# Kernel tuning notes

Hardware: AMD Instinct MI355X
Metric: run time of the kernel (lower is better)

Reference implementation:

```python
import jax, jax.numpy as jnp
import numpy as np

B, NC, A, C, G = 8, 6, 25200, 10, 20  # batch, cameras, anchors, classes, GT per camera
MAX_GT = 32                            # padded GT slots per camera (>= max num_gt)
LAMBDA_COORD, LAMBDA_NOOBJ, LAMBDA_OBJ, LAMBDA_CLS = 5.0, 0.5, 1.0, 1.0
IOU_THR = 0.5


def setup_inputs() -> dict:
    key = jax.random.key(0)
    k1, k2, k3, k4, k5, k6, k7 = jax.random.split(key, 7)
    cams = B * NC
    gt_cxcy = jax.random.uniform(k1, (cams * G, 2), minval=0.1, maxval=0.9)
    gt_wh = jax.random.uniform(k2, (cams * G, 2), minval=0.05, maxval=0.3)
    gt_boxes = jnp.concatenate([gt_cxcy, gt_wh], axis=-1)           # (960, 4) cxcywh, normalized
    gt_labels = jax.random.randint(k3, (cams * G,), 0, C)            # (960,)
    # per-sample cumulative end indices: [20, 40, ..., 120] per row
    start_end_idx = jnp.tile((jnp.arange(NC) + 1) * G, (B, 1)).astype(jnp.int32)
    pred_boxes = jax.random.uniform(k4, (cams, A, 4))
    # overlay noisy copies of the GT boxes on the first G anchors so positives exist
    noise = 0.01 * jax.random.normal(k5, (cams, G, 4))
    pred_boxes = pred_boxes.at[:, :G, :].set(gt_boxes.reshape(cams, G, 4) + noise)
    pred_labels = jax.random.normal(k6, (cams, A, C))
    pred_objectness = jax.random.normal(k7, (cams, A, 1))
    return {
        'pred_boxes': pred_boxes,
        'pred_labels': pred_labels,
        'pred_objectness': pred_objectness,
        'gt_boxes': gt_boxes,
        'gt_labels': gt_labels,
        'start_end_idx': start_end_idx,
    }


def _iou_cxcywh(pb, gb):
    # pb: (cams, A, 4), gb: (cams, MG, 4) -> (cams, A, MG)
    p = pb[:, :, None, :]
    g = gb[:, None, :, :]
    p1, p2 = p[..., :2] - p[..., 2:] * 0.5, p[..., :2] + p[..., 2:] * 0.5
    g1, g2 = g[..., :2] - g[..., 2:] * 0.5, g[..., :2] + g[..., 2:] * 0.5
    wh = jnp.clip(jnp.minimum(p2, g2) - jnp.maximum(p1, g1), 0.0)
    inter = wh[..., 0] * wh[..., 1]
    area_p = p[..., 2] * p[..., 3]
    area_g = g[..., 2] * g[..., 3]
    return inter / (area_p + area_g - inter + 1e-6)


def _safe_mean(x, mask):
    # per-camera mean over masked anchors; 0 if mask empty. x, mask: (cams, A)
    cnt = mask.sum(-1)
    s = (x * mask).sum(-1)
    return jnp.where(cnt > 0, s / jnp.maximum(cnt, 1.0), 0.0)


def reference(pred_boxes, pred_labels, pred_objectness, gt_boxes, gt_labels, start_end_idx):
    cams = pred_boxes.shape[0]
    s = start_end_idx.astype(jnp.int32)                              # (B, NC) per-sample cumulative
    offsets = jnp.concatenate([jnp.zeros((1,), jnp.int32), jnp.cumsum(s[:, -1])])[:-1]  # (B,)
    starts = (offsets[:, None] + jnp.concatenate(
        [jnp.zeros((s.shape[0], 1), jnp.int32), s[:, :-1]], axis=1)).reshape(-1)        # (cams,)
    ends = (offsets[:, None] + s).reshape(-1)                        # (cams,)
    ngt = ends - starts                                              # (cams,)

    k = jnp.arange(MAX_GT, dtype=jnp.int32)
    gidx = starts[:, None] + k[None, :]                              # (cams, MG)
    valid = k[None, :] < ngt[:, None]                                # (cams, MG)
    gidx_c = jnp.clip(gidx, 0, gt_boxes.shape[0] - 1)
    gtb = gt_boxes[gidx_c]                                           # (cams, MG, 4)
    gtl = gt_labels[gidx_c]                                          # (cams, MG)

    iou = _iou_cxcywh(pred_boxes, gtb)                               # (cams, A, MG)
    iou = jnp.where(valid[:, None, :], iou, -1.0)
    best_iou = iou.max(-1)                                           # (cams, A)
    best_gt = iou.argmax(-1)                                         # (cams, A)

    has_gt = ngt > 0
    pos = ((best_iou > IOU_THR) & has_gt[:, None]).astype(pred_boxes.dtype)  # (cams, A)
    neg = 1.0 - pos
    num_pos = pos.sum()
    num_neg = neg.sum()

    cam_ix = jnp.arange(cams)[:, None]
    matched_box = gtb[cam_ix, best_gt]                               # (cams, A, 4)
    matched_lbl = gtl[cam_ix, best_gt]                               # (cams, A)

    # box loss: per-camera sum of squared errors over positives, lambda_coord weighted
    box_se = ((pred_boxes - matched_box) ** 2).sum(-1)               # (cams, A)
    box_loss_c = LAMBDA_COORD * (box_se * pos).sum(-1)               # (cams,)

    # objectness BCE-with-logits: target 1 -> softplus(-x); target 0 -> softplus(x)
    o = pred_objectness[..., 0]                                      # (cams, A)
    obj_loss_c = LAMBDA_OBJ * _safe_mean(jax.nn.softplus(-o), pos)
    noobj_loss_c = LAMBDA_NOOBJ * _safe_mean(jax.nn.softplus(o), neg)

    # classification CE over positives (per-camera mean)
    logp = jax.nn.log_softmax(pred_labels, axis=-1)                  # (cams, A, C)
    ce = -jnp.take_along_axis(logp, matched_lbl[..., None], axis=-1)[..., 0]
    cls_loss_c = LAMBDA_CLS * _safe_mean(ce, pos)

    box_loss = jnp.where(num_pos > 0, box_loss_c.sum() / jnp.maximum(num_pos, 1.0), 0.0)
    obj_loss = jnp.where(num_pos > 0, obj_loss_c.sum() / jnp.maximum(num_pos, 1.0), 0.0)
    cls_loss = jnp.where(num_pos > 0, cls_loss_c.sum() / jnp.maximum(num_pos, 1.0), 0.0)
    noobj_loss = jnp.where(num_neg > 0, noobj_loss_c.sum() / jnp.maximum(num_neg, 1.0), 0.0)
    total_loss = box_loss + obj_loss + noobj_loss + cls_loss
    return jnp.stack([total_loss, box_loss, obj_loss, noobj_loss, cls_loss])
```

## Files before the change

### kernel.cpp

```cpp
#include <hip/hip_runtime.h>
#include <math.h>

#define NCAMS 48
#define NC_   6
#define A_    25200
#define C_    10
#define MAXGT 32
#define IOU_THR 0.5f
#define L_COORD 5.0f
#define L_NOOBJ 0.5f

#define BLOCK  256
#define APT    8
#define CHUNK  (BLOCK * APT)
#define NCHUNK ((A_ + CHUNK - 1) / CHUNK)

__device__ __forceinline__ float softplus_f(float x) {
    return fmaxf(x, 0.0f) + log1pf(expf(-fabsf(x)));
}

__global__ __launch_bounds__(BLOCK)
void yolo_phase1(const float* __restrict__ pred_boxes,
                 const float* __restrict__ pred_labels,
                 const float* __restrict__ pred_obj,
                 const float* __restrict__ gt_boxes,
                 const int*   __restrict__ gt_labels,
                 const int*   __restrict__ se,
                 int total_gt,
                 float* __restrict__ partials)
{
    const int cam   = blockIdx.y;
    const int chunk = blockIdx.x;
    const int tid   = threadIdx.x;

    __shared__ float4 s_corner[MAXGT];
    __shared__ float4 s_orig[MAXGT];
    __shared__ float  s_area[MAXGT];
    __shared__ int    s_lbl[MAXGT];
    __shared__ float  s_red[BLOCK / 64][6];

    const int b  = cam / NC_;
    const int nc = cam - b * NC_;
    int off = 0;
    for (int bb = 0; bb < b; ++bb) off += se[bb * NC_ + (NC_ - 1)];
    const int start = off + (nc ? se[b * NC_ + nc - 1] : 0);
    const int end   = off + se[b * NC_ + nc];
    int ngt = end - start;
    if (ngt < 0) ngt = 0;
    if (ngt > MAXGT) ngt = MAXGT;

    if (tid < ngt) {
        int gi = start + tid;
        gi = min(max(gi, 0), total_gt - 1);
        float4 gb = ((const float4*)gt_boxes)[gi];
        float hw = gb.z * 0.5f, hh = gb.w * 0.5f;
        s_corner[tid] = make_float4(gb.x - hw, gb.y - hh, gb.x + hw, gb.y + hh);
        s_orig[tid]   = gb;
        s_area[tid]   = gb.z * gb.w;
        s_lbl[tid]    = gt_labels[gi];
    }
    __syncthreads();

    float pos_cnt = 0.f, neg_cnt = 0.f;
    float box_acc = 0.f, spp_acc = 0.f, spn_acc = 0.f, ce_acc = 0.f;

    const int base = chunk * CHUNK;
    const float4* pb4 = (const float4*)pred_boxes;

    #pragma unroll
    for (int j = 0; j < APT; ++j) {
        const int a = base + j * BLOCK + tid;
        if (a >= A_) continue;
        const long idx = (long)cam * A_ + a;

        const float4 p = pb4[idx];
        const float phw = p.z * 0.5f, phh = p.w * 0.5f;
        const float p1x = p.x - phw, p1y = p.y - phh;
        const float p2x = p.x + phw, p2y = p.y + phh;
        const float parea = p.z * p.w;

        float best = -1.0f;
        int bk = 0;
        for (int k = 0; k < ngt; ++k) {
            const float4 g = s_corner[k];
            float wx = fminf(p2x, g.z) - fmaxf(p1x, g.x);
            float wy = fminf(p2y, g.w) - fmaxf(p1y, g.y);
            wx = fmaxf(wx, 0.0f);
            wy = fmaxf(wy, 0.0f);
            const float inter = wx * wy;
            const float iou = inter / (parea + s_area[k] - inter + 1e-6f);
            if (iou > best) { best = iou; bk = k; }
        }

        const float o = pred_obj[idx];
        if (best > IOU_THR) {
            pos_cnt += 1.0f;
            const float4 mb = s_orig[bk];
            const float dx = p.x - mb.x, dy = p.y - mb.y;
            const float dz = p.z - mb.z, dw = p.w - mb.w;
            box_acc += dx * dx + dy * dy + dz * dz + dw * dw;
            spp_acc += softplus_f(-o);
            const float* lg = pred_labels + idx * C_;
            float m = lg[0];
            #pragma unroll
            for (int i = 1; i < C_; ++i) m = fmaxf(m, lg[i]);
            float sexp = 0.f;
            #pragma unroll
            for (int i = 0; i < C_; ++i) sexp += expf(lg[i] - m);
            const int lbl = s_lbl[bk];
            ce_acc += -(lg[lbl] - m - logf(sexp));
        } else {
            neg_cnt += 1.0f;
            spn_acc += softplus_f(o);
        }
    }

    float v[6] = {pos_cnt, neg_cnt, box_acc, spp_acc, spn_acc, ce_acc};
    #pragma unroll
    for (int i = 0; i < 6; ++i) {
        float x = v[i];
        for (int s = 32; s; s >>= 1) x += __shfl_down(x, s, 64);
        v[i] = x;
    }
    if ((tid & 63) == 0) {
        const int w = tid >> 6;
        #pragma unroll
        for (int i = 0; i < 6; ++i) s_red[w][i] = v[i];
    }
    __syncthreads();
    if (tid == 0) {
        float* outp = partials + (size_t)(cam * NCHUNK + chunk) * 8;
        #pragma unroll
        for (int i = 0; i < 6; ++i)
            outp[i] = s_red[0][i] + s_red[1][i] + s_red[2][i] + s_red[3][i];
    }
}

__global__ void yolo_phase2(const float* __restrict__ partials,
                            float* __restrict__ out)
{
    const int t = threadIdx.x;
    float box_sum = 0.f, obj_sum = 0.f, noobj_sum = 0.f, cls_sum = 0.f;
    float np_ = 0.f, nn_ = 0.f;

    if (t < NCAMS) {
        float p = 0.f, n = 0.f, bx = 0.f, sp = 0.f, sn = 0.f, ce = 0.f;
        for (int h = 0; h < NCHUNK; ++h) {
            const float* q = partials + (size_t)(t * NCHUNK + h) * 8;
            p  += q[0]; n  += q[1]; bx += q[2];
            sp += q[3]; sn += q[4]; ce += q[5];
        }
        box_sum   = L_COORD * bx;
        obj_sum   = (p > 0.f) ? sp / fmaxf(p, 1.0f) : 0.f;
        cls_sum   = (p > 0.f) ? ce / fmaxf(p, 1.0f) : 0.f;
        noobj_sum = L_NOOBJ * ((n > 0.f) ? sn / fmaxf(n, 1.0f) : 0.f);
        np_ = p; nn_ = n;
    }
    for (int s = 32; s; s >>= 1) {
        box_sum   += __shfl_down(box_sum, s, 64);
        obj_sum   += __shfl_down(obj_sum, s, 64);
        noobj_sum += __shfl_down(noobj_sum, s, 64);
        cls_sum   += __shfl_down(cls_sum, s, 64);
        np_       += __shfl_down(np_, s, 64);
        nn_       += __shfl_down(nn_, s, 64);
    }
    if (t == 0) {
        const float box_loss   = (np_ > 0.f) ? box_sum / fmaxf(np_, 1.0f) : 0.f;
        const float obj_loss   = (np_ > 0.f) ? obj_sum / fmaxf(np_, 1.0f) : 0.f;
        const float cls_loss   = (np_ > 0.f) ? cls_sum / fmaxf(np_, 1.0f) : 0.f;
        const float noobj_loss = (nn_ > 0.f) ? noobj_sum / fmaxf(nn_, 1.0f) : 0.f;
        const float total = box_loss + obj_loss + noobj_loss + cls_loss;
        out[0] = total;
        out[1] = box_loss;
        out[2] = obj_loss;
        out[3] = noobj_loss;
        out[4] = cls_loss;
    }
}

extern "C" void kernel_launch(void* const* d_in, const int* in_sizes, int n_in,
                              void* d_out, int out_size, void* d_ws, size_t ws_size,
                              hipStream_t stream) {
    const float* pred_boxes  = (const float*)d_in[0];
    const float* pred_labels = (const float*)d_in[1];
    const float* pred_obj    = (const float*)d_in[2];
    const float* gt_boxes    = (const float*)d_in[3];
    const int*   gt_labels   = (const int*)d_in[4];
    const int*   se          = (const int*)d_in[5];
    const int total_gt = in_sizes[3] / 4;

    float* partials = (float*)d_ws;

    dim3 grid(NCHUNK, NCAMS);
    yolo_phase1<<<grid, BLOCK, 0, stream>>>(pred_boxes, pred_labels, pred_obj,
                                            gt_boxes, gt_labels, se,
                                            total_gt, partials);
    yolo_phase2<<<1, 64, 0, stream>>>(partials, (float*)d_out);
}
```

Measured before the change: 143.5 us.

## Shrink per-thread anchor work, interleave two anchors, specialize GT loop, use fast reciprocal

Each block now covers two anchors per thread instead of eight, which multiplies the number of blocks and raises the parallelism across CUs. Both anchors' loads are issued up front, and their IoU loops are interleaved for ILP. A fully unrolled path is added for exactly 20 GTs, and the division is replaced with the hardware approximate reciprocal. The trade-offs are more partials for phase 2 to reduce, plus a small change in IoU precision near the threshold.

```diff
diff --git a/kernel.cpp b/kernel.cpp
--- a/kernel.cpp
+++ b/kernel.cpp
@@ -11,8 +11,7 @@
 #define L_NOOBJ 0.5f
 
 #define BLOCK  256
-#define APT    8
-#define CHUNK  (BLOCK * APT)
+#define CHUNK  (BLOCK * 2)
 #define NCHUNK ((A_ + CHUNK - 1) / CHUNK)
 
 __device__ __forceinline__ float softplus_f(float x) {
@@ -61,38 +60,60 @@
     }
     __syncthreads();
 
+    const int base = chunk * CHUNK;
+    const int a0 = base + tid;
+    const int a1 = base + BLOCK + tid;
+    const bool valid0 = (a0 < A_);
+    const bool valid1 = (a1 < A_);
+    const int a0c = valid0 ? a0 : (A_ - 1);
+    const int a1c = valid1 ? a1 : (A_ - 1);
+    const long long idx0 = (long long)cam * A_ + a0c;
+    const long long idx1 = (long long)cam * A_ + a1c;
+
+    const float4* pb4 = (const float4*)pred_boxes;
+    const float4 p0 = pb4[idx0];
+    const float4 p1 = pb4[idx1];
+    const float o0 = pred_obj[idx0];
+    const float o1 = pred_obj[idx1];
+
+    const float p1x0 = p0.x - p0.z * 0.5f, p1y0 = p0.y - p0.w * 0.5f;
+    const float p2x0 = p0.x + p0.z * 0.5f, p2y0 = p0.y + p0.w * 0.5f;
+    const float pa0  = p0.z * p0.w + 1e-6f;
+    const float p1x1 = p1.x - p1.z * 0.5f, p1y1 = p1.y - p1.w * 0.5f;
+    const float p2x1 = p1.x + p1.z * 0.5f, p2y1 = p1.y + p1.w * 0.5f;
+    const float pa1  = p1.z * p1.w + 1e-6f;
+
+    float best0 = -1.0f, best1 = -1.0f;
+    int bk0 = 0, bk1 = 0;
+
+    auto iou_step = [&](int k) {
+        const float4 g = s_corner[k];
+        const float ga = s_area[k];
+        float wx0 = fmaxf(fminf(p2x0, g.z) - fmaxf(p1x0, g.x), 0.0f);
+        float wy0 = fmaxf(fminf(p2y0, g.w) - fmaxf(p1y0, g.y), 0.0f);
+        float wx1 = fmaxf(fminf(p2x1, g.z) - fmaxf(p1x1, g.x), 0.0f);
+        float wy1 = fmaxf(fminf(p2y1, g.w) - fmaxf(p1y1, g.y), 0.0f);
+        const float inter0 = wx0 * wy0;
+        const float inter1 = wx1 * wy1;
+        const float iou0 = inter0 * __builtin_amdgcn_rcpf(pa0 + (ga - inter0));
+        const float iou1 = inter1 * __builtin_amdgcn_rcpf(pa1 + (ga - inter1));
+        if (iou0 > best0) { best0 = iou0; bk0 = k; }
+        if (iou1 > best1) { best1 = iou1; bk1 = k; }
+    };
+
+    if (ngt == 20) {
+        #pragma unroll
+        for (int k = 0; k < 20; ++k) iou_step(k);
+    } else {
+        for (int k = 0; k < ngt; ++k) iou_step(k);
+    }
+
     float pos_cnt = 0.f, neg_cnt = 0.f;
     float box_acc = 0.f, spp_acc = 0.f, spn_acc = 0.f, ce_acc = 0.f;
 
-    const int base = chunk * CHUNK;
-    const float4* pb4 = (const float4*)pred_boxes;
-
-    #pragma unroll
-    for (int j = 0; j < APT; ++j) {
-        const int a = base + j * BLOCK + tid;
-        if (a >= A_) continue;
-        const long idx = (long)cam * A_ + a;
-
-        const float4 p = pb4[idx];
-        const float phw = p.z * 0.5f, phh = p.w * 0.5f;
-        const float p1x = p.x - phw, p1y = p.y - phh;
-        const float p2x = p.x + phw, p2y = p.y + phh;
-        const float parea = p.z * p.w;
-
-        float best = -1.0f;
-        int bk = 0;
-        for (int k = 0; k < ngt; ++k) {
-            const float4 g = s_corner[k];
-            float wx = fminf(p2x, g.z) - fmaxf(p1x, g.x);
-            float wy = fminf(p2y, g.w) - fmaxf(p1y, g.y);
-            wx = fmaxf(wx, 0.0f);
-            wy = fmaxf(wy, 0.0f);
-            const float inter = wx * wy;
-            const float iou = inter / (parea + s_area[k] - inter + 1e-6f);
-            if (iou > best) { best = iou; bk = k; }
-        }
-
-        const float o = pred_obj[idx];
+    auto accumulate = [&](bool valid, float best, int bk, const float4& p,
+                          float o, long long idx) {
+        if (!valid) return;
         if (best > IOU_THR) {
             pos_cnt += 1.0f;
             const float4 mb = s_orig[bk];
@@ -113,7 +134,9 @@
             neg_cnt += 1.0f;
             spn_acc += softplus_f(o);
         }
-    }
+    };
+    accumulate(valid0, best0, bk0, p0, o0, idx0);
+    accumulate(valid1, best1, bk1, p1, o1, idx1);
 
     float v[6] = {pos_cnt, neg_cnt, box_acc, spp_acc, spn_acc, ce_acc};
     #pragma unroll
```

Result: faster. 124.0 us (-13.6%).

## Interchange IoU loops, compare IoU by cross-multiplication, and specialize for 20 GTs

Applied to the files above, without the earlier changes.

Swaps the IoU loop nest so each GT box is read from shared memory once and tested against several anchors held in registers. The per-pair division is replaced by a cross-multiplied comparison of intersection over denominator, and the threshold test becomes num > 0.5*den. A fully unrolled path is added for the common case of 20 GT boxes, and anchors per thread drop from 8 to 4, doubling the block count. The aim is to remove divisions and shared-memory reloads; the cost is more register pressure and tie-breaking that can differ slightly from the division-based comparison.

```diff
diff --git a/kernel.cpp b/kernel.cpp
--- a/kernel.cpp
+++ b/kernel.cpp
@@ -6,12 +6,11 @@
 #define A_    25200
 #define C_    10
 #define MAXGT 32
-#define IOU_THR 0.5f
 #define L_COORD 5.0f
 #define L_NOOBJ 0.5f
 
 #define BLOCK  256
-#define APT    8
+#define APT    4
 #define CHUNK  (BLOCK * APT)
 #define NCHUNK ((A_ + CHUNK - 1) / CHUNK)
 
@@ -61,57 +60,80 @@
     }
     __syncthreads();
 
-    float pos_cnt = 0.f, neg_cnt = 0.f;
-    float box_acc = 0.f, spp_acc = 0.f, spn_acc = 0.f, ce_acc = 0.f;
-
     const int base = chunk * CHUNK;
     const float4* pb4 = (const float4*)pred_boxes;
+
+    int   aidx[APT];
+    bool  valid[APT];
+    float p1x[APT], p1y[APT], p2x[APT], p2y[APT], pa[APT];
+    float bn[APT], bd[APT];
+    int   bk[APT];
+    float o[APT];
+    float4 p[APT];
 
     #pragma unroll
     for (int j = 0; j < APT; ++j) {
         const int a = base + j * BLOCK + tid;
-        if (a >= A_) continue;
-        const long idx = (long)cam * A_ + a;
-
-        const float4 p = pb4[idx];
-        const float phw = p.z * 0.5f, phh = p.w * 0.5f;
-        const float p1x = p.x - phw, p1y = p.y - phh;
-        const float p2x = p.x + phw, p2y = p.y + phh;
-        const float parea = p.z * p.w;
-
-        float best = -1.0f;
-        int bk = 0;
-        for (int k = 0; k < ngt; ++k) {
-            const float4 g = s_corner[k];
-            float wx = fminf(p2x, g.z) - fmaxf(p1x, g.x);
-            float wy = fminf(p2y, g.w) - fmaxf(p1y, g.y);
-            wx = fmaxf(wx, 0.0f);
-            wy = fmaxf(wy, 0.0f);
+        valid[j] = (a < A_);
+        const int ac = valid[j] ? a : (A_ - 1);
+        const int idx = cam * A_ + ac;
+        aidx[j] = idx;
+        p[j] = pb4[idx];
+        o[j] = pred_obj[idx];
+        const float hw = p[j].z * 0.5f, hh = p[j].w * 0.5f;
+        p1x[j] = p[j].x - hw; p1y[j] = p[j].y - hh;
+        p2x[j] = p[j].x + hw; p2y[j] = p[j].y + hh;
+        pa[j]  = p[j].z * p[j].w + 1e-6f;
+        bn[j] = -1.0f; bd[j] = 1.0f; bk[j] = 0;
+    }
+
+    auto iou_step = [&](int k) {
+        const float4 g = s_corner[k];
+        const float ga = s_area[k];
+        #pragma unroll
+        for (int j = 0; j < APT; ++j) {
+            const float wx = fmaxf(fminf(p2x[j], g.z) - fmaxf(p1x[j], g.x), 0.0f);
+            const float wy = fmaxf(fminf(p2y[j], g.w) - fmaxf(p1y[j], g.y), 0.0f);
             const float inter = wx * wy;
-            const float iou = inter / (parea + s_area[k] - inter + 1e-6f);
-            if (iou > best) { best = iou; bk = k; }
+            const float d = pa[j] + (ga - inter);
+            const bool better = inter * bd[j] > bn[j] * d;
+            bn[j] = better ? inter : bn[j];
+            bd[j] = better ? d     : bd[j];
+            bk[j] = better ? k     : bk[j];
         }
-
-        const float o = pred_obj[idx];
-        if (best > IOU_THR) {
+    };
+
+    if (ngt == 20) {
+        #pragma unroll
+        for (int k = 0; k < 20; ++k) iou_step(k);
+    } else {
+        for (int k = 0; k < ngt; ++k) iou_step(k);
+    }
+
+    float pos_cnt = 0.f, neg_cnt = 0.f;
+    float box_acc = 0.f, spp_acc = 0.f, spn_acc = 0.f, ce_acc = 0.f;
+
+    #pragma unroll
+    for (int j = 0; j < APT; ++j) {
+        if (!valid[j]) continue;
+        if (bn[j] > 0.5f * bd[j]) {
             pos_cnt += 1.0f;
-            const float4 mb = s_orig[bk];
-            const float dx = p.x - mb.x, dy = p.y - mb.y;
-            const float dz = p.z - mb.z, dw = p.w - mb.w;
+            const float4 mb = s_orig[bk[j]];
+            const float dx = p[j].x - mb.x, dy = p[j].y - mb.y;
+            const float dz = p[j].z - mb.z, dw = p[j].w - mb.w;
             box_acc += dx * dx + dy * dy + dz * dz + dw * dw;
-            spp_acc += softplus_f(-o);
-            const float* lg = pred_labels + idx * C_;
+            spp_acc += softplus_f(-o[j]);
+            const float* lg = pred_labels + aidx[j] * C_;
             float m = lg[0];
             #pragma unroll
             for (int i = 1; i < C_; ++i) m = fmaxf(m, lg[i]);
             float sexp = 0.f;
             #pragma unroll
             for (int i = 0; i < C_; ++i) sexp += expf(lg[i] - m);
-            const int lbl = s_lbl[bk];
-            ce_acc += -(lg[lbl] - m - logf(sexp));
+            ce_acc += -(lg[s_lbl[bk[j]]] - m - logf(sexp));
         } else {
             neg_cnt += 1.0f;
-            spn_acc += softplus_f(o);
+            spn_acc += softplus_f(o[j]);
         }
     }
 
@@ -144,17 +166,17 @@
     float np_ = 0.f, nn_ = 0.f;
 
     if (t < NCAMS) {
-        float p = 0.f, n = 0.f, bx = 0.f, sp = 0.f, sn = 0.f, ce = 0.f;
+        float pp = 0.f, n = 0.f, bx = 0.f, sp = 0.f, sn = 0.f, ce = 0.f;
         for (int h = 0; h < NCHUNK; ++h) {
             const float* q = partials + (size_t)(t * NCHUNK + h) * 8;
-            p  += q[0]; n  += q[1]; bx += q[2];
+            pp += q[0]; n  += q[1]; bx += q[2];
             sp += q[3]; sn += q[4]; ce += q[5];
         }
         box_sum   = L_COORD * bx;
-        obj_sum   = (p > 0.f) ? sp / fmaxf(p, 1.0f) : 0.f;
-        cls_sum   = (p > 0.f) ? ce / fmaxf(p, 1.0f) : 0.f;
+        obj_sum   = (pp > 0.f) ? sp / fmaxf(pp, 1.0f) : 0.f;
+        cls_sum   = (pp > 0.f) ? ce / fmaxf(pp, 1.0f) : 0.f;
         noobj_sum = L_NOOBJ * ((n > 0.f) ? sn / fmaxf(n, 1.0f) : 0.f);
-        np_ = p; nn_ = n;
+        np_ = pp; nn_ = n;
     }
     for (int s = 32; s; s >>= 1) {
         box_sum   += __shfl_down(box_sum, s, 64);
```

Measured after the change: 124.7 us. 1.15x faster.

## Precompute GT boxes in prep kernel and use division-free IoU threshold test

Applied to the files above, without the earlier changes.

Adds a small prep kernel that writes per-camera GT corners and padded areas, plus start and count, to workspace, so each phase1 block no longer walks the start_end table or fills shared memory. The IoU>0.5 test becomes 3*inter - (area_g+eps) > area_p, max-reduced over GTs, which removes the per-GT division. The argmax with division is recomputed only for positive anchors. Anchors per thread drop from 8 to 2, giving more blocks, and the loop is fully unrolled for the 20-GT case. The cost is an extra kernel launch, GT reads from global memory instead of LDS, and a threshold test that can disagree with the reference on near-0.5 ties.

```diff
diff --git a/kernel.cpp b/kernel.cpp
--- a/kernel.cpp
+++ b/kernel.cpp
@@ -6,12 +6,11 @@
 #define A_    25200
 #define C_    10
 #define MAXGT 32
-#define IOU_THR 0.5f
 #define L_COORD 5.0f
 #define L_NOOBJ 0.5f
 
 #define BLOCK  256
-#define APT    8
+#define APT    2
 #define CHUNK  (BLOCK * APT)
 #define NCHUNK ((A_ + CHUNK - 1) / CHUNK)
 
@@ -19,25 +18,16 @@
     return fmaxf(x, 0.0f) + log1pf(expf(-fabsf(x)));
 }
 
-__global__ __launch_bounds__(BLOCK)
-void yolo_phase1(const float* __restrict__ pred_boxes,
-                 const float* __restrict__ pred_labels,
-                 const float* __restrict__ pred_obj,
-                 const float* __restrict__ gt_boxes,
-                 const int*   __restrict__ gt_labels,
-                 const int*   __restrict__ se,
-                 int total_gt,
-                 float* __restrict__ partials)
+__global__ void yolo_prep(const float* __restrict__ gt_boxes,
+                          const int*   __restrict__ se,
+                          int total_gt,
+                          float* __restrict__ gtprep,
+                          int*   __restrict__ gtmeta)
 {
-    const int cam   = blockIdx.y;
-    const int chunk = blockIdx.x;
-    const int tid   = threadIdx.x;
-
-    __shared__ float4 s_corner[MAXGT];
-    __shared__ float4 s_orig[MAXGT];
-    __shared__ float  s_area[MAXGT];
-    __shared__ int    s_lbl[MAXGT];
-    __shared__ float  s_red[BLOCK / 64][6];
+    const int t   = blockIdx.x * blockDim.x + threadIdx.x;
+    const int cam = t >> 5;
+    const int k   = t & 31;
+    if (cam >= NCAMS) return;
 
     const int b  = cam / NC_;
     const int nc = cam - b * NC_;
@@ -46,74 +36,121 @@
     const int start = off + (nc ? se[b * NC_ + nc - 1] : 0);
     const int end   = off + se[b * NC_ + nc];
     int ngt = end - start;
-    if (ngt < 0) ngt = 0;
-    if (ngt > MAXGT) ngt = MAXGT;
-
-    if (tid < ngt) {
-        int gi = start + tid;
-        gi = min(max(gi, 0), total_gt - 1);
-        float4 gb = ((const float4*)gt_boxes)[gi];
-        float hw = gb.z * 0.5f, hh = gb.w * 0.5f;
-        s_corner[tid] = make_float4(gb.x - hw, gb.y - hh, gb.x + hw, gb.y + hh);
-        s_orig[tid]   = gb;
-        s_area[tid]   = gb.z * gb.w;
-        s_lbl[tid]    = gt_labels[gi];
-    }
-    __syncthreads();
+    ngt = min(max(ngt, 0), MAXGT);
+
+    if (k == 0) { gtmeta[cam * 2] = start; gtmeta[cam * 2 + 1] = ngt; }
+    float* q = gtprep + (size_t)(cam * MAXGT + k) * 8;
+    if (k < ngt) {
+        const int gi = min(max(start + k, 0), total_gt - 1);
+        const float4 gb = ((const float4*)gt_boxes)[gi];
+        const float hw = gb.z * 0.5f, hh = gb.w * 0.5f;
+        q[0] = gb.x - hw; q[1] = gb.y - hh;
+        q[2] = gb.x + hw; q[3] = gb.y + hh;
+        q[4] = gb.z * gb.w + 1e-6f;
+    }
+}
+
+__global__ __launch_bounds__(BLOCK)
+void yolo_phase1(const float* __restrict__ pred_boxes,
+                 const float* __restrict__ pred_labels,
+                 const float* __restrict__ pred_obj,
+                 const float* __restrict__ gt_boxes,
+                 const int*   __restrict__ gt_labels,
+                 const float* __restrict__ gtprep,
+                 const int*   __restrict__ gtmeta,
+                 int total_gt,
+                 float* __restrict__ partials)
+{
+    const int cam   = blockIdx.y;
+    const int chunk = blockIdx.x;
+    const int tid   = threadIdx.x;
+
+    __shared__ float s_red[BLOCK / 64][6];
+
+    const int start = gtmeta[cam * 2];
+    const int ngt   = gtmeta[cam * 2 + 1];
+    const float* __restrict__ gp = gtprep + (size_t)cam * MAXGT * 8;
+
+    const int base = chunk * CHUNK;
+    const float4* pb4 = (const float4*)pred_boxes;
+
+    const int a0 = base + tid;
+    const int a1 = base + BLOCK + tid;
+    const bool v0 = (a0 < A_);
+    const bool v1 = (a1 < A_);
+    const int idx0 = cam * A_ + (v0 ? a0 : (A_ - 1));
+    const int idx1 = cam * A_ + (v1 ? a1 : (A_ - 1));
+
+    const float4 p0 = pb4[idx0];
+    const float4 p1 = pb4[idx1];
+    const float o0 = pred_obj[idx0];
+    const float o1 = pred_obj[idx1];
+
+    const float p1x0 = p0.x - p0.z * 0.5f, p1y0 = p0.y - p0.w * 0.5f;
+    const float p2x0 = p0.x + p0.z * 0.5f, p2y0 = p0.y + p0.w * 0.5f;
+    const float pa0  = p0.z * p0.w;
+    const float p1x1 = p1.x - p1.z * 0.5f, p1y1 = p1.y - p1.w * 0.5f;
+    const float p2x1 = p1.x + p1.z * 0.5f, p2y1 = p1.y + p1.w * 0.5f;
+    const float pa1  = p1.z * p1.w;
+
+    float m0 = -1e30f, m1 = -1e30f;
+    auto step = [&](int k) {
+        const float g1x = gp[k * 8 + 0], g1y = gp[k * 8 + 1];
+        const float g2x = gp[k * 8 + 2], g2y = gp[k * 8 + 3];
+        const float thr = gp[k * 8 + 4];
+        const float wx0 = fmaxf(fminf(p2x0, g2x) - fmaxf(p1x0, g1x), 0.0f);
+        const float wy0 = fmaxf(fminf(p2y0, g2y) - fmaxf(p1y0, g1y), 0.0f);
+        const float wx1 = fmaxf(fminf(p2x1, g2x) - fmaxf(p1x1, g1x), 0.0f);
+        const float wy1 = fmaxf(fminf(p2y1, g2y) - fmaxf(p1y1, g1y), 0.0f);
+        m0 = fmaxf(m0, fmaf(3.0f, wx0 * wy0, -thr));
+        m1 = fmaxf(m1, fmaf(3.0f, wx1 * wy1, -thr));
+    };
+    if (ngt == 20) {
+        #pragma unroll
+        for (int k = 0; k < 20; ++k) step(k);
+    } else {
+        for (int k = 0; k < ngt; ++k) step(k);
+    }
 
     float pos_cnt = 0.f, neg_cnt = 0.f;
     float box_acc = 0.f, spp_acc = 0.f, spn_acc = 0.f, ce_acc = 0.f;
 
-    const int base = chunk * CHUNK;
-    const float4* pb4 = (const float4*)pred_boxes;
-
-    #pragma unroll
-    for (int j = 0; j < APT; ++j) {
-        const int a = base + j * BLOCK + tid;
-        if (a >= A_) continue;
-        const long idx = (long)cam * A_ + a;
-
-        const float4 p = pb4[idx];
-        const float phw = p.z * 0.5f, phh = p.w * 0.5f;
-        const float p1x = p.x - phw, p1y = p.y - phh;
-        const float p2x = p.x + phw, p2y = p.y + phh;
-        const float parea = p.z * p.w;
-
-        float best = -1.0f;
-        int bk = 0;
-        for (int k = 0; k < ngt; ++k) {
-            const float4 g = s_corner[k];
-            float wx = fminf(p2x, g.z) - fmaxf(p1x, g.x);
-            float wy = fminf(p2y, g.w) - fmaxf(p1y, g.y);
-            wx = fmaxf(wx, 0.0f);
-            wy = fmaxf(wy, 0.0f);
-            const float inter = wx * wy;
-            const float iou = inter / (parea + s_area[k] - inter + 1e-6f);
-            if (iou > best) { best = iou; bk = k; }
-        }
-
-        const float o = pred_obj[idx];
-        if (best > IOU_THR) {
+    auto handle = [&](bool valid, float m, float pa, const float4& p,
+                      float p1x, float p1y, float p2x, float p2y,
+                      float o, int idx) {
+        if (!valid) return;
+        if (m > pa) {
             pos_cnt += 1.0f;
-            const float4 mb = s_orig[bk];
-            const float dx = p.x - mb.x, dy = p.y - mb.y;
-            const float dz = p.z - mb.z, dw = p.w - mb.w;
+            float best = -1.0f; int bk = 0;
+            for (int k = 0; k < ngt; ++k) {
+                const float wx = fmaxf(fminf(p2x, gp[k*8+2]) - fmaxf(p1x, gp[k*8+0]), 0.0f);
+                const float wy = fmaxf(fminf(p2y, gp[k*8+3]) - fmaxf(p1y, gp[k*8+1]), 0.0f);
+                const float inter = wx * wy;
+                const float den = pa + (gp[k*8+4] - inter);
+                const float iou = inter / den;
+                if (iou > best) { best = iou; bk = k; }
+            }
+            const int gi = min(max(start + bk, 0), total_gt - 1);
+            const float4 gb = ((const float4*)gt_boxes)[gi];
+            const float dx = p.x - gb.x, dy = p.y - gb.y;
+            const float dz = p.z - gb.z, dw = p.w - gb.w;
             box_acc += dx * dx + dy * dy + dz * dz + dw * dw;
             spp_acc += softplus_f(-o);
-            const float* lg = pred_labels + idx * C_;
-            float m = lg[0];
+            const float* lg = pred_labels + (size_t)idx * C_;
+            float mx = lg[0];
             #pragma unroll
-            for (int i = 1; i < C_; ++i) m = fmaxf(m, lg[i]);
+            for (int i = 1; i < C_; ++i) mx = fmaxf(mx, lg[i]);
             float sexp = 0.f;
             #pragma unroll
-            for (int i = 0; i < C_; ++i) sexp += expf(lg[i] - m);
-            const int lbl = s_lbl[bk];
-            ce_acc += -(lg[lbl] - m - logf(sexp));
+            for (int i = 0; i < C_; ++i) sexp += expf(lg[i] - mx);
+            ce_acc += -(lg[gt_labels[gi]] - mx - logf(sexp));
         } else {
             neg_cnt += 1.0f;
             spn_acc += softplus_f(o);
         }
-    }
+    };
+    handle(v0, m0, pa0, p0, p1x0, p1y0, p2x0, p2y0, o0, idx0);
+    handle(v1, m1, pa1, p1, p1x1, p1y1, p2x1, p2y1, o1, idx1);
 
     float v[6] = {pos_cnt, neg_cnt, box_acc, spp_acc, spn_acc, ce_acc};
     #pragma unroll
@@ -144,17 +181,17 @@
     float np_ = 0.f, nn_ = 0.f;
 
     if (t < NCAMS) {
-        float p = 0.f, n = 0.f, bx = 0.f, sp = 0.f, sn = 0.f, ce = 0.f;
+        float pp = 0.f, n = 0.f, bx = 0.f, sp = 0.f, sn = 0.f, ce = 0.f;
         for (int h = 0; h < NCHUNK; ++h) {
             const float* q = partials + (size_t)(t * NCHUNK + h) * 8;
-            p  += q[0]; n  += q[1]; bx += q[2];
+            pp += q[0]; n  += q[1]; bx += q[2];
             sp += q[3]; sn += q[4]; ce += q[5];
         }
         box_sum   = L_COORD * bx;
-        obj_sum   = (p > 0.f) ? sp / fmaxf(p, 1.0f) : 0.f;
-        cls_sum   = (p > 0.f) ? ce / fmaxf(p, 1.0f) : 0.f;
+        obj_sum   = (pp > 0.f) ? sp / fmaxf(pp, 1.0f) : 0.f;
+        cls_sum   = (pp > 0.f) ? ce / fmaxf(pp, 1.0f) : 0.f;
         noobj_sum = L_NOOBJ * ((n > 0.f) ? sn / fmaxf(n, 1.0f) : 0.f);
-        np_ = p; nn_ = n;
+        np_ = pp; nn_ = n;
     }
     for (int s = 32; s; s >>= 1) {
         box_sum   += __shfl_down(box_sum, s, 64);
@@ -190,10 +227,15 @@
     const int total_gt = in_sizes[3] / 4;
 
     float* partials = (float*)d_ws;
+    float* gtprep   = partials + (size_t)NCAMS * NCHUNK * 8;
+    int*   gtmeta   = (int*)(gtprep + (size_t)NCAMS * MAXGT * 8);
+
+    yolo_prep<<<(NCAMS * 32 + 255) / 256, 256, 0, stream>>>(
+        gt_boxes, se, total_gt, gtprep, gtmeta);
 
     dim3 grid(NCHUNK, NCAMS);
     yolo_phase1<<<grid, BLOCK, 0, stream>>>(pred_boxes, pred_labels, pred_obj,
-                                            gt_boxes, gt_labels, se,
-                                            total_gt, partials);
+                                            gt_boxes, gt_labels,
+                                            gtprep, gtmeta, total_gt, partials);
     yolo_phase2<<<1, 64, 0, stream>>>(partials, (float*)d_out);
 }
```

Result: faster. 133.0 us (-7.3%).
